# Kernel optimization log

Hardware: AMD Instinct MI355X
Metric: run time of the kernel (lower is better)

## Reference

```python
import jax, jax.numpy as jnp
import numpy as np

EPS = 1e-8


def setup_inputs() -> dict:
    key = jax.random.key(0)
    ks = jax.random.split(key, 3)
    B, d_in, d_sae = 2048, 2048, 16384
    x = jax.random.normal(ks[0], (B, 2, d_in), dtype=jnp.float32)
    W_enc = jax.random.normal(ks[1], (d_in, d_sae), dtype=jnp.float32) / (d_in ** 0.5)
    W_dec = jax.random.normal(ks[2], (d_sae, d_in), dtype=jnp.float32) / (d_sae ** 0.5)
    b_enc = jnp.zeros((d_sae,), dtype=jnp.float32)
    b_dec = jnp.zeros((d_in,), dtype=jnp.float32)
    return {"x": x, "W_enc": W_enc, "W_dec": W_dec, "b_enc": b_enc,
            "b_dec": b_dec, "k": 64, "h": 8192}


def _encode(x, W_enc, b_enc, k):
    # x: (N, d_in) -> z: (N, d_sae), top-k sparsified with relu on kept values
    pre = x @ W_enc + b_enc
    v, i = jax.lax.top_k(pre, k)                       # (N, k)
    rows = jnp.arange(pre.shape[0])[:, None]
    return jnp.zeros_like(pre).at[rows, i].set(jax.nn.relu(v))


def _info_nce(z_a, z_b):
    z_a = z_a / jnp.maximum(jnp.linalg.norm(z_a, axis=-1, keepdims=True), EPS)
    z_b = z_b / jnp.maximum(jnp.linalg.norm(z_b, axis=-1, keepdims=True), EPS)
    sim = z_a @ z_b.T                                  # (B, B)
    diag = jnp.diagonal(sim)
    ce_row = jnp.mean(jax.nn.logsumexp(sim, axis=1) - diag)
    ce_col = jnp.mean(jax.nn.logsumexp(sim, axis=0) - diag)
    return 0.5 * (ce_row + ce_col)


def reference(x, W_enc, W_dec, b_enc, b_dec, k, h):
    alpha = 1.0
    B, _, d_in = x.shape
    # encode both tokens in one GEMM: (2B, d_in)
    x_flat = x.reshape(B * 2, d_in)
    z = _encode(x_flat, W_enc, b_enc, k)               # (2B, d_sae)
    x_hat_full = z @ W_dec + b_dec                     # (2B, d_in)
    x_hat_high = z[:, :h] @ W_dec[:h, :] + b_dec       # (2B, d_in)
    per_tok = d_in
    # mean over batch per token, summed over prev+cur (matches 4 separate means)
    se_full = jnp.sum((x_hat_full - x_flat) ** 2, axis=-1).reshape(B, 2)
    se_high = jnp.sum((x_hat_high - x_flat) ** 2, axis=-1).reshape(B, 2)
    l_matr = (jnp.mean(se_full, axis=0).sum() + jnp.mean(se_high, axis=0).sum()) / per_tok
    z2 = z.reshape(B, 2, -1)
    z_h_prev = z2[:, 0, :h]
    z_h_cur = z2[:, 1, :h]
    l_contr = _info_nce(z_h_cur, z_h_prev)
    total = l_matr + alpha * l_contr
    x_hat_cur = x_hat_full.reshape(B, 2, d_in)[:, 1]
    z_cur = z2[:, 1]
    return (total, x_hat_cur, z_cur)
```

## Files before the change

kernel.cpp:

```cpp
#include <hip/hip_runtime.h>
#include <hip/hip_bf16.h>
#include <math.h>

#define D_IN   2048
#define D_SAE  16384
#define NROWS  4096
#define KTOP   64
#define HDIM   8192
#define CHUNK  1024
#define EPSN   1e-8f
#define BANDW_F16 4e-3f
#define BANDW_F32 4e-4f
#define BANDCAP 512
#define NTILE   128
#define SEG     16
#define CAPT    (NTILE*SEG)
#define TH_CAND 2.0f

typedef unsigned short u16;
typedef unsigned char u8;
typedef _Float16 f16;
typedef __attribute__((ext_vector_type(8))) _Float16 f16x8;
typedef __attribute__((ext_vector_type(4))) _Float16 f16x4;
typedef __attribute__((ext_vector_type(8))) unsigned short u16x8;
typedef __attribute__((ext_vector_type(4))) float float4v;
typedef __attribute__((ext_vector_type(2))) float f32x2;

__device__ __forceinline__ unsigned f2u(float f) {
  unsigned b = __float_as_uint(f);
  return (b & 0x80000000u) ? ~b : (b | 0x80000000u);
}
__device__ __forceinline__ float u2f(unsigned u) {
  unsigned b = (u & 0x80000000u) ? (u & 0x7fffffffu) : ~u;
  return __uint_as_float(b);
}
__device__ __forceinline__ u16 f2bf_rne(float f) {
  unsigned b = __float_as_uint(f);
  unsigned r = (b + 0x7fffu + ((b >> 16) & 1u)) >> 16;
  return (u16)r;
}
__device__ __forceinline__ float bf2f(u16 u) {
  return __uint_as_float(((unsigned)u) << 16);
}
__device__ __forceinline__ void async_copy16(void* lds, const void* g) {
  __builtin_amdgcn_global_load_lds(
      (const __attribute__((address_space(1))) unsigned*)(g),
      (__attribute__((address_space(3))) unsigned*)(lds), 16, 0, 0);
}

__global__ __launch_bounds__(256)
void pre_kernel(const float* __restrict__ x, const float* __restrict__ W,
                f16* __restrict__ Axh, f16* __restrict__ Th,
                float* __restrict__ WT)
{
  __shared__ float S[64][65];
  const int bid = blockIdx.x;
  if (bid < 8192) {
    const int tx = threadIdx.x & 63, ty = threadIdx.x >> 6;
    const int n0 = (bid & 255) * 64, k0 = (bid >> 8) * 64;
#pragma unroll
    for (int i = 0; i < 16; ++i) {
      int kl = ty + i * 4;
      S[kl][tx] = W[(size_t)(k0 + kl) * D_SAE + n0 + tx];
    }
    __syncthreads();
#pragma unroll
    for (int i = 0; i < 16; ++i) {
      int nl = ty + i * 4;
      float v = S[tx][nl];
      Th[(size_t)(n0 + nl) * D_IN + k0 + tx] = (f16)v;
      WT[(size_t)(n0 + nl) * D_IN + k0 + tx] = v;
    }
  } else {
    int t = (bid - 8192) * 256 + threadIdx.x;
    const int n4 = (NROWS * D_IN) / 4;
    if (t < n4) {
      float4 v = ((const float4*)x)[t];
      f16x4 h;
      h.x = (f16)v.x; h.y = (f16)v.y; h.z = (f16)v.z; h.w = (f16)v.w;
      ((f16x4*)Axh)[t] = h;
    }
  }
}

__global__ __launch_bounds__(512, 2)
void gemm_f16_kernel(const f16* __restrict__ Axh,
                     const f16* __restrict__ BT,
                     const float* __restrict__ bias,
                     unsigned* __restrict__ ckey_g,
                     u16* __restrict__ cidx_g,
                     unsigned* __restrict__ ccnt)
{
  __shared__ u16 As[2][2][256 * 32];
  __shared__ u16 Bs[2][2][256 * 32];
  const int tid  = threadIdx.x;
  const int wave = tid >> 6, lane = tid & 63;
  const int bid  = blockIdx.x;
  const int xcd  = bid & 7, loc = bid >> 3;
  const int n0   = (xcd * 8 + (loc >> 4)) * 256;
  const int m0   = (loc & 15) * 256;
  const int wr   = wave >> 2;
  const int wc   = wave & 3;
  const int fr   = lane & 15;
  const int fsl  = lane >> 4;

  float4v acc[8][4];
#pragma unroll
  for (int i = 0; i < 8; ++i)
#pragma unroll
    for (int j = 0; j < 4; ++j) acc[i][j] = (float4v){0.f, 0.f, 0.f, 0.f};

  int aoff[8], boff[4];
#pragma unroll
  for (int mi = 0; mi < 8; ++mi) {
    int row = wr * 128 + mi * 16 + fr;
    aoff[mi] = row * 32 + ((fsl ^ ((row >> 1) & 3)) * 8);
  }
#pragma unroll
  for (int n = 0; n < 4; ++n) {
    int col = wc * 64 + n * 16 + fr;
    boff[n] = col * 32 + ((fsl ^ ((col >> 1) & 3)) * 8);
  }

  auto stA = [&](int bf, int tt, int ks, int half) {
    int idx = half * 512 + tid;
    int row = idx >> 2, sl = idx & 3;
    int gc = tt * 64 + ks * 32 + ((sl ^ ((row >> 1) & 3)) * 8);
    async_copy16((char*)&As[bf][ks][0] + (size_t)idx * 16,
                 Axh + (size_t)(m0 + row) * D_IN + gc);
  };
  auto stB = [&](int bf, int tt, int ks, int half) {
    int idx = half * 512 + tid;
    int row = idx >> 2, sl = idx & 3;
    int gc = tt * 64 + ks * 32 + ((sl ^ ((row >> 1) & 3)) * 8);
    async_copy16((char*)&Bs[bf][ks][0] + (size_t)idx * 16,
                 BT + (size_t)(n0 + row) * D_IN + gc);
  };

  stA(0, 0, 0, 0); stA(0, 0, 0, 1); stB(0, 0, 0, 0); stB(0, 0, 0, 1);
  stA(0, 0, 1, 0); stA(0, 0, 1, 1); stB(0, 0, 1, 0); stB(0, 0, 1, 1);
  asm volatile("s_waitcnt vmcnt(4)" ::: "memory");
  __builtin_amdgcn_s_barrier();

  for (int t = 0; t < 32; ++t) {
    const int buf = t & 1, nbf = buf ^ 1;
    const bool st = (t < 31);
#pragma unroll
    for (int ks = 0; ks < 2; ++ks) {
      const u16* Ak = &As[buf][ks][0];
      const u16* Bk = &Bs[buf][ks][0];
      f16x8 b0 = *(const f16x8*)&Bk[boff[0]];
      f16x8 b1 = *(const f16x8*)&Bk[boff[1]];
      f16x8 b2 = *(const f16x8*)&Bk[boff[2]];
      f16x8 b3 = *(const f16x8*)&Bk[boff[3]];
      f16x8 a0 = *(const f16x8*)&Ak[aoff[0]];
      f16x8 a1 = *(const f16x8*)&Ak[aoff[1]];
      f16x8 a2 = *(const f16x8*)&Ak[aoff[2]];
      f16x8 a3 = *(const f16x8*)&Ak[aoff[3]];
      if (st) { stA(nbf, t + 1, ks, 0); stA(nbf, t + 1, ks, 1); }
      __builtin_amdgcn_s_setprio(1);
      acc[0][0] = __builtin_amdgcn_mfma_f32_16x16x32_f16(a0, b0, acc[0][0], 0, 0, 0);
      acc[0][1] = __builtin_amdgcn_mfma_f32_16x16x32_f16(a0, b1, acc[0][1], 0, 0, 0);
      acc[0][2] = __builtin_amdgcn_mfma_f32_16x16x32_f16(a0, b2, acc[0][2], 0, 0, 0);
      acc[0][3] = __builtin_amdgcn_mfma_f32_16x16x32_f16(a0, b3, acc[0][3], 0, 0, 0);
      acc[1][0] = __builtin_amdgcn_mfma_f32_16x16x32_f16(a1, b0, acc[1][0], 0, 0, 0);
      acc[1][1] = __builtin_amdgcn_mfma_f32_16x16x32_f16(a1, b1, acc[1][1], 0, 0, 0);
      acc[1][2] = __builtin_amdgcn_mfma_f32_16x16x32_f16(a1, b2, acc[1][2], 0, 0, 0);
      acc[1][3] = __builtin_amdgcn_mfma_f32_16x16x32_f16(a1, b3, acc[1][3], 0, 0, 0);
      acc[2][0] = __builtin_amdgcn_mfma_f32_16x16x32_f16(a2, b0, acc[2][0], 0, 0, 0);
      acc[2][1] = __builtin_amdgcn_mfma_f32_16x16x32_f16(a2, b1, acc[2][1], 0, 0, 0);
      acc[2][2] = __builtin_amdgcn_mfma_f32_16x16x32_f16(a2, b2, acc[2][2], 0, 0, 0);
      acc[2][3] = __builtin_amdgcn_mfma_f32_16x16x32_f16(a2, b3, acc[2][3], 0, 0, 0);
      acc[3][0] = __builtin_amdgcn_mfma_f32_16x16x32_f16(a3, b0, acc[3][0], 0, 0, 0);
      acc[3][1] = __builtin_amdgcn_mfma_f32_16x16x32_f16(a3, b1, acc[3][1], 0, 0, 0);
      acc[3][2] = __builtin_amdgcn_mfma_f32_16x16x32_f16(a3, b2, acc[3][2], 0, 0, 0);
      acc[3][3] = __builtin_amdgcn_mfma_f32_16x16x32_f16(a3, b3, acc[3][3], 0, 0, 0);
      __builtin_amdgcn_s_setprio(0);
      a0 = *(const f16x8*)&Ak[aoff[4]];
      a1 = *(const f16x8*)&Ak[aoff[5]];
      a2 = *(const f16x8*)&Ak[aoff[6]];
      a3 = *(const f16x8*)&Ak[aoff[7]];
      if (st) { stB(nbf, t + 1, ks, 0); stB(nbf, t + 1, ks, 1); }
      __builtin_amdgcn_s_setprio(1);
      acc[4][0] = __builtin_amdgcn_mfma_f32_16x16x32_f16(a0, b0, acc[4][0], 0, 0, 0);
      acc[4][1] = __builtin_amdgcn_mfma_f32_16x16x32_f16(a0, b1, acc[4][1], 0, 0, 0);
      acc[4][2] = __builtin_amdgcn_mfma_f32_16x16x32_f16(a0, b2, acc[4][2], 0, 0, 0);
      acc[4][3] = __builtin_amdgcn_mfma_f32_16x16x32_f16(a0, b3, acc[4][3], 0, 0, 0);
      acc[5][0] = __builtin_amdgcn_mfma_f32_16x16x32_f16(a1, b0, acc[5][0], 0, 0, 0);
      acc[5][1] = __builtin_amdgcn_mfma_f32_16x16x32_f16(a1, b1, acc[5][1], 0, 0, 0);
      acc[5][2] = __builtin_amdgcn_mfma_f32_16x16x32_f16(a1, b2, acc[5][2], 0, 0, 0);
      acc[5][3] = __builtin_amdgcn_mfma_f32_16x16x32_f16(a1, b3, acc[5][3], 0, 0, 0);
      acc[6][0] = __builtin_amdgcn_mfma_f32_16x16x32_f16(a2, b0, acc[6][0], 0, 0, 0);
      acc[6][1] = __builtin_amdgcn_mfma_f32_16x16x32_f16(a2, b1, acc[6][1], 0, 0, 0);
      acc[6][2] = __builtin_amdgcn_mfma_f32_16x16x32_f16(a2, b2, acc[6][2], 0, 0, 0);
      acc[6][3] = __builtin_amdgcn_mfma_f32_16x16x32_f16(a2, b3, acc[6][3], 0, 0, 0);
      acc[7][0] = __builtin_amdgcn_mfma_f32_16x16x32_f16(a3, b0, acc[7][0], 0, 0, 0);
      acc[7][1] = __builtin_amdgcn_mfma_f32_16x16x32_f16(a3, b1, acc[7][1], 0, 0, 0);
      acc[7][2] = __builtin_amdgcn_mfma_f32_16x16x32_f16(a3, b2, acc[7][2], 0, 0, 0);
      acc[7][3] = __builtin_amdgcn_mfma_f32_16x16x32_f16(a3, b3, acc[7][3], 0, 0, 0);
      __builtin_amdgcn_s_setprio(0);
      if (st) {
        asm volatile("s_waitcnt vmcnt(4)" ::: "memory");
        __builtin_amdgcn_s_barrier();
      } else if (ks == 0) {
        asm volatile("s_waitcnt vmcnt(0)" ::: "memory");
        __builtin_amdgcn_s_barrier();
      }
    }
  }
  __syncthreads();

  unsigned* lcnt = (unsigned*)&As[0][0][0];
  lcnt[tid] = 0u;
  __syncthreads();
  const int tl = wc >> 1;
  const int tileG = (n0 >> 7) + tl;
  const int orow = (lane >> 4) * 4;
#pragma unroll
  for (int mi = 0; mi < 8; ++mi) {
#pragma unroll
    for (int nj = 0; nj < 4; ++nj) {
      int col = n0 + wc * 64 + nj * 16 + fr;
      float bv = bias[col];
#pragma unroll
      for (int rr = 0; rr < 4; ++rr) {
        float val = acc[mi][nj][rr] + bv;
        if (val >= TH_CAND) {
          int lrow = wr * 128 + mi * 16 + orow + rr;
          unsigned j = atomicAdd(&lcnt[tl * 256 + lrow], 1u);
          if (j < SEG) {
            size_t sb = ((size_t)(m0 + lrow) * NTILE + tileG) * SEG;
            ckey_g[sb + j] = f2u(val);
            cidx_g[sb + j] = (u16)col;
          }
        }
      }
    }
  }
  __syncthreads();
  ccnt[(size_t)(m0 + (tid & 255)) * NTILE + (n0 >> 7) + (tid >> 8)] = lcnt[tid];
}

__global__ __launch_bounds__(256)
void select_compact_kernel(const unsigned* __restrict__ ckey_g,
                           const u16* __restrict__ cidx_g,
                           const unsigned* __restrict__ ccnt,
                           const float* __restrict__ x,
                           const float* __restrict__ WT,
                           const float* __restrict__ benc,
                           float bandw,
                           int*   __restrict__ topk_idx,
                           float* __restrict__ topk_val,
                           float* __restrict__ nh_norm,
                           unsigned* __restrict__ flags)
{
  __shared__ unsigned ckey[CAPT];
  __shared__ u16      cidx[CAPT];
  __shared__ unsigned tof[128];
  __shared__ unsigned tc[128];
  __shared__ unsigned hist[256];
  __shared__ unsigned sscan[257];
  __shared__ unsigned wsum[4];
  __shared__ float    bv_l[64];
  __shared__ int      band_idx[BANDCAP];
  __shared__ float    band_val[BANDCAP];
  __shared__ double   band_ex[BANDCAP];
  __shared__ unsigned char picked[BANDCAP];
  __shared__ int      out_idx[64];
  __shared__ float    out_val[64];
  __shared__ float    sh_v64;
  __shared__ unsigned sh_mcnt, sh_bstar, sh_kth, sh_ocnt, sh_bcnt, sh_bad;

  const int tid = threadIdx.x;
  const int wv = tid >> 6, ln = tid & 63;
  const int r = blockIdx.x;

  if (tid == 0) { sh_ocnt = 0u; sh_bcnt = 0u; sh_bad = 0u; sh_mcnt = 0u; sh_bstar = 0xffffffffu; }
  hist[tid] = 0u;
  if (tid < 128) {
    unsigned c = ccnt[(size_t)r * NTILE + tid];
    tc[tid] = c;
    if (c > SEG) sh_bad = 1u;
  }
  __syncthreads();
  if (tid < 128) {
    unsigned v = tc[tid];
#pragma unroll
    for (int d = 1; d < 64; d <<= 1) {
      unsigned t = __shfl_up(v, d);
      if (ln >= d) v += t;
    }
    tof[tid] = v;
  }
  __syncthreads();
  if (tid >= 64 && tid < 128) tof[tid] += tof[63];
  __syncthreads();
  const unsigned cc_u = tof[127];
  const int cc = (int)(cc_u < CAPT ? cc_u : CAPT);

  {
    unsigned ck[8]; u16 ci[8]; unsigned pv[8];
#pragma unroll
    for (int b = 0; b < 8; ++b) {
      int idx = tid + 256 * b;
      int tile = idx >> 4, slot = idx & 15;
      unsigned c = tc[tile]; if (c > SEG) c = SEG;
      bool valid = (unsigned)slot < c;
      pv[b] = valid ? (tof[tile] - tc[tile] + slot) : 0xffffffffu;
      ck[b] = valid ? ckey_g[(size_t)r * CAPT + idx] : 0u;
      ci[b] = valid ? cidx_g[(size_t)r * CAPT + idx] : (u16)0;
    }
#pragma unroll
    for (int b = 0; b < 8; ++b) {
      if (pv[b] < (unsigned)CAPT) { ckey[pv[b]] = ck[b]; cidx[pv[b]] = ci[b]; }
    }
  }
  __syncthreads();

  bool bad = (sh_bad != 0u) || (cc_u < 64u) || (cc_u > (unsigned)CAPT);

  if (!bad) {
    for (int s = tid; s < cc; s += 256) {
      float v = u2f(ckey[s]);
      int b = (int)((v - TH_CAND) * 100.0f);
      b = b < 0 ? 0 : (b > 255 ? 255 : b);
      atomicAdd(&hist[b], 1u);
    }
  }
  __syncthreads();
  {
    int rt = 255 - tid;
    unsigned v = hist[rt];
#pragma unroll
    for (int d = 1; d < 64; d <<= 1) {
      unsigned t = __shfl_up(v, d);
      if (ln >= d) v += t;
    }
    if (ln == 63) wsum[wv] = v;
    __syncthreads();
    unsigned add = 0;
    for (int w = 0; w < wv; ++w) add += wsum[w];
    sscan[rt] = v + add;
    if (tid == 0) sscan[256] = 0u;
    __syncthreads();
    if (sscan[tid] >= 64u && sscan[tid + 1] < 64u) {
      sh_bstar = (unsigned)tid;
      sh_kth = 64u - sscan[tid + 1];
    }
  }
  __syncthreads();

  if (bad || sh_bstar == 0xffffffffu) { if (tid == 0) flags[r] = 1u; return; }
  const int bstar = (int)sh_bstar;
  const unsigned kth = sh_kth;

  for (int s = tid; s < cc; s += 256) {
    float v = u2f(ckey[s]);
    int b = (int)((v - TH_CAND) * 100.0f);
    b = b < 0 ? 0 : (b > 255 ? 255 : b);
    if (b == bstar) {
      unsigned p = atomicAdd(&sh_mcnt, 1u);
      if (p < 64u) bv_l[p] = v;
    }
  }
  __syncthreads();
  if (sh_mcnt > 64u) { if (tid == 0) flags[r] = 1u; return; }
  const int m = (int)sh_mcnt;
  if (wv == 0 && ln < m) {
    float mine = bv_l[ln];
    int rank = 0;
    for (int j = 0; j < m; ++j) {
      float o = bv_l[j];
      if (o > mine || (o == mine && j < ln)) ++rank;
    }
    if (rank == (int)kth - 1) sh_v64 = mine;
  }
  __syncthreads();
  const float v64 = sh_v64;

  const float hi = v64 + 2.f * bandw, lo = v64 - 2.f * bandw;
  for (int s = tid; s < cc; s += 256) {
    float v = u2f(ckey[s]);
    int i = (int)cidx[s];
    if (v > hi) {
      unsigned p = atomicAdd(&sh_ocnt, 1u);
      out_idx[p] = i; out_val[p] = v;
    } else if (v >= lo) {
      unsigned p = atomicAdd(&sh_bcnt, 1u);
      if (p < BANDCAP) { band_idx[p] = i; band_val[p] = v; }
    }
  }
  __syncthreads();
  if (sh_bcnt > BANDCAP) { if (tid == 0) flags[r] = 1u; return; }
  const unsigned nci = sh_ocnt;
  const unsigned bcnt = sh_bcnt;
  const unsigned remaining = 64u - nci;

  if (bcnt == remaining) {
    for (unsigned s = tid; s < bcnt; s += 256) {
      out_idx[nci + s] = band_idx[s];
      out_val[nci + s] = band_val[s];
    }
    __syncthreads();
  } else {
    const float* xr = x + (size_t)r * 2048;
    for (unsigned bi = wv; bi < bcnt; bi += 4) {
      int c = band_idx[bi];
      const float* wr = WT + (size_t)c * 2048;
      double s = 0.0;
      for (int j0 = 0; j0 < 2048; j0 += 512) {
        float xa[8], wa[8];
#pragma unroll
        for (int u = 0; u < 8; ++u) {
          int j = j0 + ln + 64 * u;
          xa[u] = xr[j];
          wa[u] = wr[j];
        }
#pragma unroll
        for (int u = 0; u < 8; ++u)
          s += (double)xa[u] * (double)wa[u];
      }
#pragma unroll
      for (int off2 = 32; off2 > 0; off2 >>= 1)
        s += __shfl_down(s, off2);
      if (ln == 0) band_ex[bi] = s + (double)benc[c];
    }
    __syncthreads();
    if (tid == 0) {
      for (unsigned i2 = 0; i2 < bcnt; ++i2) picked[i2] = 0;
      for (unsigned s = 0; s < remaining; ++s) {
        int best = -1;
        for (unsigned b2 = 0; b2 < bcnt; ++b2) {
          if (picked[b2]) continue;
          if (best < 0 || band_ex[b2] > band_ex[best] ||
              (band_ex[b2] == band_ex[best] && band_idx[b2] < band_idx[best]))
            best = (int)b2;
        }
        picked[best] = 1;
        out_idx[nci + s] = band_idx[best];
        out_val[nci + s] = (float)band_ex[best];
      }
    }
    __syncthreads();
  }

  if (tid < 64) {
    float v = out_val[tid];
    v = v > 0.f ? v : 0.f;
    out_val[tid] = v;
    topk_idx[(size_t)r * 64 + tid] = out_idx[tid];
    topk_val[(size_t)r * 64 + tid] = v;
  }
  __syncthreads();
  if (tid == 0) {
    float n2 = 0.f;
    for (int s = 0; s < 64; ++s)
      if (out_idx[s] < HDIM) n2 += out_val[s] * out_val[s];
    nh_norm[r] = sqrtf(n2);
    flags[r] = 0u;
  }
}

__global__ __launch_bounds__(256)
void repair_kernel(const unsigned* __restrict__ flags,
                   const float* __restrict__ x,
                   const float* __restrict__ WT,
                   const float* __restrict__ benc,
                   int* __restrict__ topk_idx,
                   float* __restrict__ topk_val,
                   float* __restrict__ nh_norm)
{
  const int r = blockIdx.x;
  if (flags[r] == 0u) return;
  __shared__ float prerow[16384];
  __shared__ float xs[2048];
  __shared__ float rv[256];
  __shared__ int   ri[256];
  __shared__ int   oi[64];
  __shared__ float ov[64];
  const int tid = threadIdx.x;
  for (int i = tid; i < 2048; i += 256) xs[i] = x[(size_t)r * 2048 + i];
  __syncthreads();
  for (int c = tid; c < 16384; c += 256) {
    const float* wr = WT + (size_t)c * 2048;
    float s = 0.f;
    for (int j = 0; j < 2048; ++j) s = fmaf(xs[j], wr[j], s);
    prerow[c] = s + benc[c];
  }
  __syncthreads();
  for (int k2 = 0; k2 < 64; ++k2) {
    float bv = -INFINITY; int bi = 16384;
    for (int c = tid; c < 16384; c += 256) {
      float v = prerow[c];
      if (v > bv || (v == bv && c < bi)) { bv = v; bi = c; }
    }
    rv[tid] = bv; ri[tid] = bi;
    __syncthreads();
    for (int s2 = 128; s2 > 0; s2 >>= 1) {
      if (tid < s2) {
        if (rv[tid+s2] > rv[tid] || (rv[tid+s2] == rv[tid] && ri[tid+s2] < ri[tid])) {
          rv[tid] = rv[tid+s2]; ri[tid] = ri[tid+s2];
        }
      }
      __syncthreads();
    }
    if (tid == 0) { oi[k2] = ri[0]; ov[k2] = rv[0]; prerow[ri[0]] = -INFINITY; }
    __syncthreads();
  }
  if (tid < 64) {
    float v = ov[tid]; v = v > 0.f ? v : 0.f;
    topk_idx[(size_t)r * 64 + tid] = oi[tid];
    topk_val[(size_t)r * 64 + tid] = v;
  }
  __syncthreads();
  if (tid == 0) {
    float n2 = 0.f;
    for (int s = 0; s < 64; ++s)
      if (oi[s] < HDIM) { float v = ov[s] > 0.f ? ov[s] : 0.f; n2 += v * v; }
    nh_norm[r] = sqrtf(n2);
  }
}

__global__ __launch_bounds__(256)
void wdec_scatter_kernel(const float* __restrict__ W,
                         u8* __restrict__ W8, float* __restrict__ scl,
                         const int* __restrict__ topk_idx,
                         const float* __restrict__ topk_val,
                         const float* __restrict__ nh_norm,
                         u16* __restrict__ ZpTb)
{
  const int bid = blockIdx.x;
  const int tid = threadIdx.x;
  if (bid < 16384) {
    __shared__ float red[256];
    const int c = bid;
    const int e0 = tid * 8;
    const float* wr = W + (size_t)c * 2048;
    float4 a = *(const float4*)(wr + e0);
    float4 b = *(const float4*)(wr + e0 + 4);
    float w[8] = {a.x,a.y,a.z,a.w,b.x,b.y,b.z,b.w};
    float mx = 0.f;
#pragma unroll
    for (int i = 0; i < 8; ++i) mx = fmaxf(mx, fabsf(w[i]));
    red[tid] = mx; __syncthreads();
    for (int s = 128; s > 0; s >>= 1) { if (tid < s) red[tid] = fmaxf(red[tid], red[tid+s]); __syncthreads(); }
    const float mxa = red[0];
    const float senc = mxa > 0.f ? 448.f / mxa : 0.f;
    float q[8];
#pragma unroll
    for (int i = 0; i < 8; ++i) q[i] = fminf(fmaxf(w[i] * senc, -448.f), 448.f);
    int p0 = __builtin_amdgcn_cvt_pk_fp8_f32(q[0], q[1], 0, false);
    p0 = __builtin_amdgcn_cvt_pk_fp8_f32(q[2], q[3], p0, true);
    int p1 = __builtin_amdgcn_cvt_pk_fp8_f32(q[4], q[5], 0, false);
    p1 = __builtin_amdgcn_cvt_pk_fp8_f32(q[6], q[7], p1, true);
    uint2 o; o.x = (unsigned)p0; o.y = (unsigned)p1;
    *(uint2*)(W8 + (size_t)c * 2048 + e0) = o;
    if (tid == 0) scl[c] = mxa > 0.f ? mxa / 448.f : 0.f;
  } else {
    int t = (bid - 16384) * 256 + tid;
    if (t < 2048 * 64) {
      int b = t >> 6;
      int r = 2 * b;
      int c = topk_idx[(size_t)r * 64 + (t & 63)];
      float v = topk_val[(size_t)r * 64 + (t & 63)];
      if (c < HDIM) {
        float nrm = nh_norm[r]; nrm = nrm > EPSN ? nrm : EPSN;
        ZpTb[(size_t)c * 2048 + b] = f2bf_rne(v / nrm);
      }
    }
  }
}

__global__ __launch_bounds__(256)
void token_kernel(const int* __restrict__ topk_idx,
                  const float* __restrict__ topk_val,
                  const u8* __restrict__ W8,
                  const float* __restrict__ scl,
                  const float* __restrict__ bdec,
                  const float* __restrict__ x,
                  const float* __restrict__ nh_norm,
                  const u16* __restrict__ ZpTb,
                  float* __restrict__ se_full,
                  float* __restrict__ se_high,
                  float* __restrict__ xhat_out,
                  float* __restrict__ zcur_out,
                  float* __restrict__ simb,
                  float* __restrict__ lse_row,
                  float* __restrict__ diag)
{
  __shared__ int sidx[64];
  __shared__ float sval[64];
  __shared__ float rawv[64];
  __shared__ float red[256];
  __shared__ int cidx2[64];
  __shared__ float cval2[64];
  __shared__ u8 zmap[16384];
  __shared__ int scnt;
  const int tid = threadIdx.x;
  const int r = blockIdx.x;
  const int e0 = tid * 8;
  const bool odd = (r & 1);
  if (tid == 0) scnt = 0;
  if (odd) {
    unsigned* zm = (unsigned*)zmap;
#pragma unroll
    for (int j = 0; j < 16; ++j) zm[tid + 256 * j] = 0xFFFFFFFFu;
  }
  if (tid < 64) {
    int c = topk_idx[(size_t)r*64+tid];
    float v = topk_val[(size_t)r*64+tid];
    sidx[tid] = c;
    rawv[tid] = v;
    sval[tid] = v * scl[c];
  }
  __syncthreads();
  if (odd && tid < 64) zmap[sidx[tid]] = (u8)tid;
  float accf[8], acch[8];
  {
    float4 b0 = *(const float4*)(bdec + e0);
    float4 b1 = *(const float4*)(bdec + e0 + 4);
    accf[0]=b0.x; accf[1]=b0.y; accf[2]=b0.z; accf[3]=b0.w;
    accf[4]=b1.x; accf[5]=b1.y; accf[6]=b1.z; accf[7]=b1.w;
#pragma unroll
    for (int i = 0; i < 8; ++i) acch[i] = accf[i];
  }
  for (int s0 = 0; s0 < 64; s0 += 8) {
    uint2 w[8]; float vf[8], vh[8];
#pragma unroll
    for (int j = 0; j < 8; ++j) {
      int c = sidx[s0 + j];
      float v = sval[s0 + j];
      vf[j] = v;
      vh[j] = (c < HDIM) ? v : 0.f;
      w[j] = *(const uint2*)(W8 + (size_t)c * 2048 + e0);
    }
#pragma unroll
    for (int j = 0; j < 8; ++j) {
      f32x2 f0 = __builtin_amdgcn_cvt_pk_f32_fp8((int)w[j].x, false);
      f32x2 f1 = __builtin_amdgcn_cvt_pk_f32_fp8((int)w[j].x, true);
      f32x2 f2 = __builtin_amdgcn_cvt_pk_f32_fp8((int)w[j].y, false);
      f32x2 f3 = __builtin_amdgcn_cvt_pk_f32_fp8((int)w[j].y, true);
      float wvv[8] = {f0[0],f0[1],f1[0],f1[1],f2[0],f2[1],f3[0],f3[1]};
#pragma unroll
      for (int i = 0; i < 8; ++i) {
        accf[i] = fmaf(vf[j], wvv[i], accf[i]);
        acch[i] = fmaf(vh[j], wvv[i], acch[i]);
      }
    }
  }
  const float* xr = x + (size_t)r * 2048;
  float4 x0 = *(const float4*)(xr + e0);
  float4 x1 = *(const float4*)(xr + e0 + 4);
  float xv[8] = {x0.x,x0.y,x0.z,x0.w,x1.x,x1.y,x1.z,x1.w};
  float sf = 0.f, shs = 0.f;
#pragma unroll
  for (int i = 0; i < 8; ++i) {
    float df = accf[i] - xv[i]; sf += df*df;
    float dh = acch[i] - xv[i]; shs += dh*dh;
  }
  red[tid] = sf; __syncthreads();
  for (int s2=128; s2>0; s2>>=1){ if (tid<s2) red[tid]+=red[tid+s2]; __syncthreads(); }
  if (tid==0) se_full[r] = red[0];
  __syncthreads();
  red[tid] = shs; __syncthreads();
  for (int s2=128; s2>0; s2>>=1){ if (tid<s2) red[tid]+=red[tid+s2]; __syncthreads(); }
  if (tid==0) se_high[r] = red[0];
  if (!odd) return;

  {
    float* orow = xhat_out + (size_t)(r >> 1) * 2048;
    float4 o0 = {accf[0],accf[1],accf[2],accf[3]};
    float4 o1 = {accf[4],accf[5],accf[6],accf[7]};
    *(float4*)(orow + e0) = o0;
    *(float4*)(orow + e0 + 4) = o1;
  }
  {
    float* zrow = zcur_out + (size_t)(r >> 1) * 16384;
#pragma unroll
    for (int it = 0; it < 16; ++it) {
      int c0 = it * 1024 + tid * 4;
      float4 o;
      u8 s0m = zmap[c0 + 0]; o.x = (s0m < 64) ? rawv[s0m] : 0.f;
      u8 s1m = zmap[c0 + 1]; o.y = (s1m < 64) ? rawv[s1m] : 0.f;
      u8 s2m = zmap[c0 + 2]; o.z = (s2m < 64) ? rawv[s2m] : 0.f;
      u8 s3m = zmap[c0 + 3]; o.w = (s3m < 64) ? rawv[s3m] : 0.f;
      *(float4*)(zrow + c0) = o;
    }
  }
  const int i = r >> 1;
  __syncthreads();
  if (tid < 64) {
    int c = sidx[tid];
    float v = rawv[tid];
    if (c < HDIM) {
      float nrm = nh_norm[r]; nrm = nrm > EPSN ? nrm : EPSN;
      int p = atomicAdd(&scnt, 1);
      cidx2[p] = c; cval2[p] = v / nrm;
    }
  }
  __syncthreads();
  float acc[8];
#pragma unroll
  for (int ii = 0; ii < 8; ++ii) acc[ii] = 0.f;
  const int m = scnt;
  int s = 0;
  for (; s + 8 <= m; s += 8) {
    u16x8 z[8]; float vv[8];
#pragma unroll
    for (int j = 0; j < 8; ++j) {
      vv[j] = cval2[s + j];
      z[j] = *(const u16x8*)(ZpTb + (size_t)cidx2[s + j] * 2048 + e0);
    }
#pragma unroll
    for (int j = 0; j < 8; ++j)
#pragma unroll
      for (int ii = 0; ii < 8; ++ii)
        acc[ii] = fmaf(vv[j], bf2f(z[j][ii]), acc[ii]);
  }
  for (; s < m; ++s) {
    int c = cidx2[s]; float v = cval2[s];
    u16x8 z8 = *(const u16x8*)(ZpTb + (size_t)c * 2048 + e0);
#pragma unroll
    for (int ii = 0; ii < 8; ++ii)
      acc[ii] = fmaf(v, bf2f(z8[ii]), acc[ii]);
  }
  {
    float* srow = simb + (size_t)i * 2048;
    float4 o0 = {acc[0],acc[1],acc[2],acc[3]};
    float4 o1 = {acc[4],acc[5],acc[6],acc[7]};
    *(float4*)(srow + e0) = o0;
    *(float4*)(srow + e0 + 4) = o1;
  }
  float mx = -INFINITY;
#pragma unroll
  for (int ii = 0; ii < 8; ++ii) mx = fmaxf(mx, acc[ii]);
  if ((i >> 3) == tid) diag[i] = acc[i & 7];
  red[tid] = mx; __syncthreads();
  for (int s2=128; s2>0; s2>>=1){ if (tid<s2) red[tid]=fmaxf(red[tid],red[tid+s2]); __syncthreads(); }
  mx = red[0]; __syncthreads();
  float se = 0.f;
#pragma unroll
  for (int ii = 0; ii < 8; ++ii) se += expf(acc[ii] - mx);
  red[tid] = se; __syncthreads();
  for (int s2=128; s2>0; s2>>=1){ if (tid<s2) red[tid]+=red[tid+s2]; __syncthreads(); }
  if (tid == 0) lse_row[i] = mx + logf(red[0]);
}

__global__ __launch_bounds__(256)
void gemm_pre_kernel(const float* __restrict__ A,
                     const float* __restrict__ B,
                     const float* __restrict__ bias,
                     float* __restrict__ C)
{
  __shared__ float As[16][129];
  __shared__ float Bs[16][129];
  const int tid = threadIdx.x;
  const int tx = tid & 15, ty = tid >> 4;
  const int m0 = blockIdx.y * 128;
  const int n0 = blockIdx.x * 128;
  float acc[8][8];
#pragma unroll
  for (int i = 0; i < 8; ++i)
#pragma unroll
    for (int j = 0; j < 8; ++j) acc[i][j] = 0.f;
  const int lk = tid & 15, lm = tid >> 4;
  for (int k0 = 0; k0 < 2048; k0 += 16) {
#pragma unroll
    for (int i = 0; i < 8; ++i) {
      int m = lm + 16 * i;
      As[lk][m] = A[(size_t)(m0 + m) * 2048 + k0 + lk];
    }
#pragma unroll
    for (int i = 0; i < 8; ++i) {
      int idx = tid + 256 * i;
      int kk = idx >> 7, nn = idx & 127;
      Bs[kk][nn] = B[(size_t)(k0 + kk) * 16384 + n0 + nn];
    }
    __syncthreads();
#pragma unroll
    for (int kk = 0; kk < 16; ++kk) {
      float a[8], b[8];
#pragma unroll
      for (int i = 0; i < 8; ++i) a[i] = As[kk][ty + 16 * i];
#pragma unroll
      for (int j = 0; j < 8; ++j) b[j] = Bs[kk][tx + 16 * j];
#pragma unroll
      for (int i = 0; i < 8; ++i)
#pragma unroll
        for (int j = 0; j < 8; ++j) acc[i][j] = fmaf(a[i], b[j], acc[i][j]);
    }
    __syncthreads();
  }
#pragma unroll
  for (int i = 0; i < 8; ++i) {
    int m = m0 + ty + 16 * i;
#pragma unroll
    for (int j = 0; j < 8; ++j) {
      int n = n0 + tx + 16 * j;
      C[(size_t)m * 16384 + n] = acc[i][j] + bias[n];
    }
  }
}

__global__ __launch_bounds__(256)
void select_fb_kernel(const float* __restrict__ pre,
                      const float* __restrict__ x,
                      const float* __restrict__ Wenc,
                      const float* __restrict__ benc,
                      int row_base, float bandw,
                      int*   __restrict__ topk_idx,
                      float* __restrict__ topk_val,
                      float* __restrict__ nh_norm)
{
  __shared__ unsigned hist[256];
  __shared__ int      band_idx[BANDCAP];
  __shared__ double   band_ex[BANDCAP];
  __shared__ double   red_d[256];
  __shared__ int      out_idx[64];
  __shared__ float    out_val[64];
  __shared__ unsigned char picked[BANDCAP];
  __shared__ unsigned sh_prefix, sh_need, sh_ocnt, sh_bcnt;

  const int tid = threadIdx.x;
  const int lrow = blockIdx.x;
  const int row = row_base + lrow;
  const float* prow = pre + (size_t)lrow * 16384;

  if (tid == 0) { sh_prefix = 0u; sh_need = 64u; }
  __syncthreads();
  for (int level = 24; level >= 0; level -= 8) {
    hist[tid] = 0u;
    __syncthreads();
    unsigned prefix = sh_prefix;
    for (int i = tid; i < 16384; i += 256) {
      unsigned u = f2u(prow[i]);
      bool match = (level == 24) || ((u >> ((level + 8) & 31)) == prefix);
      if (match) atomicAdd(&hist[(u >> level) & 255u], 1u);
    }
    __syncthreads();
    if (tid == 0) {
      unsigned need = sh_need, acc = 0; int q = 0;
      for (int b2 = 255; b2 >= 0; --b2) {
        if (acc + hist[b2] >= need) { q = b2; break; }
        acc += hist[b2];
      }
      sh_prefix = (prefix << 8) | (unsigned)q;
      sh_need = need - acc;
    }
    __syncthreads();
  }
  const float v64 = u2f(sh_prefix);

  if (tid == 0) { sh_ocnt = 0u; sh_bcnt = 0u; }
  __syncthreads();
  const float hi = v64 + 2.f * bandw, lo = v64 - 2.f * bandw;
  for (int i = tid; i < 16384; i += 256) {
    float v = prow[i];
    if (v > hi) {
      unsigned p = atomicAdd(&sh_ocnt, 1u);
      out_idx[p] = i; out_val[p] = v;
    } else if (v >= lo) {
      unsigned p = atomicAdd(&sh_bcnt, 1u);
      if (p < BANDCAP) { band_idx[p] = i; }
    }
  }
  __syncthreads();
  const unsigned nci = sh_ocnt;
  const unsigned bcnt = sh_bcnt < BANDCAP ? sh_bcnt : BANDCAP;
  const unsigned remaining = 64u - nci;

  if (bcnt == remaining) {
    for (unsigned s = tid; s < bcnt; s += 256) {
      int c = band_idx[s];
      out_idx[nci + s] = c;
      out_val[nci + s] = prow[c];
    }
    __syncthreads();
  } else {
    const float* xr = x + (size_t)row * 2048;
    for (unsigned bi = 0; bi < bcnt; ++bi) {
      int c = band_idx[bi];
      double part = 0.0;
#pragma unroll
      for (int j2 = 0; j2 < 8; ++j2) {
        int kk = tid + 256 * j2;
        part += (double)xr[kk] * (double)Wenc[(size_t)kk * 16384 + c];
      }
      red_d[tid] = part;
      __syncthreads();
      for (int sft = 128; sft > 0; sft >>= 1) {
        if (tid < sft) red_d[tid] += red_d[tid + sft];
        __syncthreads();
      }
      if (tid == 0) band_ex[bi] = red_d[0] + (double)benc[c];
      __syncthreads();
    }
    if (tid == 0) {
      for (unsigned i2 = 0; i2 < bcnt; ++i2) picked[i2] = 0;
      for (unsigned s = 0; s < remaining; ++s) {
        int best = -1;
        for (unsigned b2 = 0; b2 < bcnt; ++b2) {
          if (picked[b2]) continue;
          if (best < 0 || band_ex[b2] > band_ex[best] ||
              (band_ex[b2] == band_ex[best] && band_idx[b2] < band_idx[best]))
            best = (int)b2;
        }
        picked[best] = 1;
        out_idx[nci + s] = band_idx[best];
        out_val[nci + s] = (float)band_ex[best];
      }
    }
    __syncthreads();
  }

  if (tid < 64) {
    float v = out_val[tid];
    v = v > 0.f ? v : 0.f;
    out_val[tid] = v;
    topk_idx[(size_t)row * 64 + tid] = out_idx[tid];
    topk_val[(size_t)row * 64 + tid] = v;
  }
  __syncthreads();
  if (tid == 0) {
    float n2 = 0.f;
    for (int s = 0; s < 64; ++s)
      if (out_idx[s] < HDIM) n2 += out_val[s] * out_val[s];
    nh_norm[row] = sqrtf(n2);
  }
}

__global__ __launch_bounds__(256)
void scatter_f32_kernel(const int* __restrict__ topk_idx,
                        const float* __restrict__ topk_val,
                        const float* __restrict__ nh_norm,
                        float* __restrict__ zcur_out,
                        float* __restrict__ ZpT)
{
  int t = blockIdx.x * blockDim.x + threadIdx.x;
  if (t >= NROWS * 64) return;
  int r = t >> 6;
  int c = topk_idx[t];
  float v = topk_val[t];
  int b = r >> 1;
  if (r & 1) {
    zcur_out[(size_t)b * 16384 + c] = v;
  } else if (c < HDIM) {
    float nrm = nh_norm[r]; nrm = nrm > EPSN ? nrm : EPSN;
    ZpT[(size_t)c * 2048 + b] = v / nrm;
  }
}

__global__ __launch_bounds__(256)
void decode_f32_kernel(const int* __restrict__ topk_idx,
                       const float* __restrict__ topk_val,
                       const float* __restrict__ Wdec,
                       const float* __restrict__ bdec,
                       const float* __restrict__ x,
                       float* __restrict__ se_full,
                       float* __restrict__ se_high,
                       float* __restrict__ xhat_out)
{
  __shared__ int sidx[64];
  __shared__ float sval[64];
  __shared__ float red[256];
  const int tid = threadIdx.x;
  const int r = blockIdx.x;
  if (tid < 64) { sidx[tid] = topk_idx[(size_t)r*64+tid]; sval[tid] = topk_val[(size_t)r*64+tid]; }
  __syncthreads();
  float accf[8], acch[8];
#pragma unroll
  for (int i = 0; i < 8; ++i) { float b = bdec[tid + 256*i]; accf[i] = b; acch[i] = b; }
  for (int s = 0; s < 64; ++s) {
    int c = sidx[s]; float v = sval[s];
    const float* wr = Wdec + (size_t)c * 2048;
    bool high = (c < HDIM);
#pragma unroll
    for (int i = 0; i < 8; ++i) {
      float w = wr[tid + 256*i];
      accf[i] = fmaf(v, w, accf[i]);
      if (high) acch[i] = fmaf(v, w, acch[i]);
    }
  }
  const float* xr = x + (size_t)r * 2048;
  float sf = 0.f, shs = 0.f;
#pragma unroll
  for (int i = 0; i < 8; ++i) {
    float xv = xr[tid + 256*i];
    float df = accf[i] - xv; sf += df*df;
    float dh = acch[i] - xv; shs += dh*dh;
  }
  red[tid] = sf; __syncthreads();
  for (int s2=128; s2>0; s2>>=1){ if (tid<s2) red[tid]+=red[tid+s2]; __syncthreads(); }
  if (tid==0) se_full[r] = red[0];
  __syncthreads();
  red[tid] = shs; __syncthreads();
  for (int s2=128; s2>0; s2>>=1){ if (tid<s2) red[tid]+=red[tid+s2]; __syncthreads(); }
  if (tid==0) se_high[r] = red[0];
  if (r & 1) {
    float* orow = xhat_out + (size_t)(r >> 1) * 2048;
#pragma unroll
    for (int i = 0; i < 8; ++i) orow[tid + 256*i] = accf[i];
  }
}

__global__ __launch_bounds__(256)
void sim_f32_kernel(const int* __restrict__ topk_idx,
                    const float* __restrict__ topk_val,
                    const float* __restrict__ nh_norm,
                    const float* __restrict__ ZpT,
                    float* __restrict__ sim)
{
  __shared__ int cidx2[64];
  __shared__ float cval2[64];
  __shared__ int scnt;
  const int tid = threadIdx.x;
  const int i = blockIdx.x;
  const int r = 2 * i + 1;
  if (tid == 0) scnt = 0;
  __syncthreads();
  if (tid < 64) {
    int c = topk_idx[(size_t)r*64+tid];
    float v = topk_val[(size_t)r*64+tid];
    if (c < HDIM) {
      float nrm = nh_norm[r]; nrm = nrm > EPSN ? nrm : EPSN;
      int p = atomicAdd(&scnt, 1);
      cidx2[p] = c; cval2[p] = v / nrm;
    }
  }
  __syncthreads();
  float acc[8];
#pragma unroll
  for (int ii = 0; ii < 8; ++ii) acc[ii] = 0.f;
  int m = scnt;
  for (int s = 0; s < m; ++s) {
    int c = cidx2[s]; float v = cval2[s];
    const float* zr = ZpT + (size_t)c * 2048;
#pragma unroll
    for (int ii = 0; ii < 8; ++ii)
      acc[ii] = fmaf(v, zr[tid + 256*ii], acc[ii]);
  }
  float* srow = sim + (size_t)i * 2048;
#pragma unroll
  for (int ii = 0; ii < 8; ++ii) srow[tid + 256*ii] = acc[ii];
}

__global__ __launch_bounds__(256)
void lse_row_kernel(const float* __restrict__ sim,
                    float* __restrict__ lse_row, float* __restrict__ diag)
{
  __shared__ float red[256];
  const int tid = threadIdx.x; const int i = blockIdx.x;
  const int e0 = tid * 8;
  const float* srow = sim + (size_t)i * 2048;
  float4 v0 = *(const float4*)(srow + e0);
  float4 v1 = *(const float4*)(srow + e0 + 4);
  float vals[8] = {v0.x,v0.y,v0.z,v0.w,v1.x,v1.y,v1.z,v1.w};
  float mx = -INFINITY;
#pragma unroll
  for (int ii=0; ii<8; ++ii) mx = fmaxf(mx, vals[ii]);
  if ((i >> 3) == tid) diag[i] = vals[i & 7];
  red[tid]=mx; __syncthreads();
  for (int s=128;s>0;s>>=1){ if (tid<s) red[tid]=fmaxf(red[tid],red[tid+s]); __syncthreads(); }
  mx = red[0]; __syncthreads();
  float se=0.f;
#pragma unroll
  for (int ii=0;ii<8;++ii) se += expf(vals[ii]-mx);
  red[tid]=se; __syncthreads();
  for (int s=128;s>0;s>>=1){ if (tid<s) red[tid]+=red[tid+s]; __syncthreads(); }
  if (tid==0) lse_row[i] = mx + logf(red[0]);
}

__global__ __launch_bounds__(256)
void lse_col_kernel(const float* __restrict__ sim, float* __restrict__ lse_col)
{
  __shared__ float ml[32][9], sl[32][9];
  const int tid = threadIdx.x;
  const int c = tid & 7, rr = tid >> 3;
  const int col = blockIdx.x * 8 + c;
  float m = -INFINITY, s = 0.f;
  for (int r = rr; r < 2048; r += 32) {
    float v = sim[(size_t)r * 2048 + col];
    float mn = fmaxf(m, v);
    s = s * expf(m - mn) + expf(v - mn);
    m = mn;
  }
  ml[rr][c] = m; sl[rr][c] = s;
  __syncthreads();
  if (rr == 0) {
    float M = ml[0][c];
#pragma unroll
    for (int i = 1; i < 32; ++i) M = fmaxf(M, ml[i][c]);
    float S = 0.f;
#pragma unroll
    for (int i = 0; i < 32; ++i) S += sl[i][c] * expf(ml[i][c] - M);
    lse_col[col] = M + logf(S);
  }
}

__global__ __launch_bounds__(256)
void final_kernel(const float* __restrict__ se_full, const float* __restrict__ se_high,
                  const float* __restrict__ lse_row, const float* __restrict__ lse_col,
                  const float* __restrict__ diag, float* __restrict__ out0)
{
  __shared__ float red[256];
  const int tid = threadIdx.x;
  float s1 = 0.f;
  for (int i = tid; i < 4096; i += 256) s1 += se_full[i] + se_high[i];
  red[tid]=s1; __syncthreads();
  for (int s=128;s>0;s>>=1){ if (tid<s) red[tid]+=red[tid+s]; __syncthreads(); }
  float matr = red[0]; __syncthreads();
  float s2 = 0.f;
  for (int i = tid; i < 2048; i += 256) s2 += (lse_row[i]-diag[i]) + (lse_col[i]-diag[i]);
  red[tid]=s2; __syncthreads();
  for (int s=128;s>0;s>>=1){ if (tid<s) red[tid]+=red[tid+s]; __syncthreads(); }
  if (tid == 0) {
    float l_matr  = matr / (2048.f * 2048.f);
    float l_contr = 0.5f * (red[0] / 2048.f);
    out0[0] = l_matr + l_contr;
  }
}

extern "C" void kernel_launch(void* const* d_in, const int* in_sizes, int n_in,
                              void* d_out, int out_size, void* d_ws, size_t ws_size,
                              hipStream_t stream)
{
  const float* x    = (const float*)d_in[0];
  const float* Wenc = (const float*)d_in[1];
  const float* Wdec = (const float*)d_in[2];
  const float* benc = (const float*)d_in[3];
  const float* bdec = (const float*)d_in[4];
  float* out = (float*)d_out;
  float* xhat_out = out + 1;
  float* zcur_out = out + 1 + (size_t)2048 * 2048;
  (void)in_sizes; (void)n_in; (void)out_size;

  char* ws = (char*)d_ws;
  size_t off = 0;
  auto alloc = [&](size_t bytes) {
    char* p = ws + off; off += (bytes + 255) & ~(size_t)255; return p;
  };
  int*      tki     = (int*)     alloc((size_t)NROWS * 64 * 4);
  float*    tkv     = (float*)   alloc((size_t)NROWS * 64 * 4);
  float*    nh_norm = (float*)   alloc((size_t)NROWS * 4);
  float*    se_f    = (float*)   alloc((size_t)NROWS * 4);
  float*    se_h    = (float*)   alloc((size_t)NROWS * 4);
  float*    lse_r   = (float*)   alloc((size_t)2048 * 4);
  float*    lse_c   = (float*)   alloc((size_t)2048 * 4);
  float*    diag    = (float*)   alloc((size_t)2048 * 4);
  f16*      Axh     = (f16*)     alloc((size_t)NROWS * D_IN * 2);
  unsigned* ckey_g  = (unsigned*)alloc((size_t)NROWS * CAPT * 4);
  u16*      cidx_g  = (u16*)     alloc((size_t)NROWS * CAPT * 2);
  unsigned* ccnt    = (unsigned*)alloc((size_t)NROWS * NTILE * 4);
  unsigned* flags   = (unsigned*)alloc((size_t)NROWS * 4);
  char*     R1      = alloc((size_t)D_SAE * D_IN * 2);
  char*     R2      = alloc((size_t)D_SAE * D_IN * 4);
  size_t need = off;

  f16*   Th    = (f16*)R1;
  u8*    W8    = (u8*)R1;
  float* scl   = (float*)(R1 + (size_t)D_SAE * D_IN);
  float* WT    = (float*)R2;
  u16*   ZpTb  = (u16*)R2;
  float* simb  = (float*)(R2 + (size_t)8192 * 2048 * 2);

  if (ws_size >= need) {
    pre_kernel<<<16384, 256, 0, stream>>>(x, Wenc, Axh, Th, WT);
    gemm_f16_kernel<<<1024, 512, 0, stream>>>(Axh, Th, benc, ckey_g, cidx_g, ccnt);
    select_compact_kernel<<<NROWS, 256, 0, stream>>>(ckey_g, cidx_g, ccnt, x, WT, benc,
        BANDW_F16, tki, tkv, nh_norm, flags);
    repair_kernel<<<NROWS, 256, 0, stream>>>(flags, x, WT, benc, tki, tkv, nh_norm);
    hipMemsetAsync(ZpTb, 0, (size_t)8192 * 2048 * 2, stream);
    wdec_scatter_kernel<<<16384 + 512, 256, 0, stream>>>(Wdec, W8, scl,
        tki, tkv, nh_norm, ZpTb);
    token_kernel<<<NROWS, 256, 0, stream>>>(tki, tkv, W8, scl, bdec, x, nh_norm, ZpTb,
        se_f, se_h, xhat_out, zcur_out, simb, lse_r, diag);
    lse_col_kernel<<<256, 256, 0, stream>>>(simb, lse_c);
    final_kernel<<<1, 256, 0, stream>>>(se_f, se_h, lse_r, lse_c, diag, out);
  } else {
    off = 0;
    float* pre2  = (float*)alloc((size_t)CHUNK * 16384 * 4);
    int*   tki2  = (int*)  alloc((size_t)NROWS * 64 * 4);
    float* tkv2  = (float*)alloc((size_t)NROWS * 64 * 4);
    float* nh2   = (float*)alloc((size_t)NROWS * 4);
    float* sef2  = (float*)alloc((size_t)NROWS * 4);
    float* seh2  = (float*)alloc((size_t)NROWS * 4);
    float* lr2   = (float*)alloc((size_t)2048 * 4);
    float* lc2   = (float*)alloc((size_t)2048 * 4);
    float* dg2   = (float*)alloc((size_t)2048 * 4);
    float* ZpT2  = (float*)alloc((size_t)8192 * 2048 * 4);
    float* sim2  = (float*)alloc((size_t)2048 * 2048 * 4);
    hipMemsetAsync(zcur_out, 0, (size_t)2048 * 16384 * 4, stream);
    for (int ch = 0; ch < 4; ++ch) {
      dim3 g(128, 8);
      gemm_pre_kernel<<<g, 256, 0, stream>>>(x + (size_t)ch * CHUNK * 2048, Wenc, benc, pre2);
      select_fb_kernel<<<CHUNK, 256, 0, stream>>>(pre2, x, Wenc, benc,
          ch * CHUNK, BANDW_F32, tki2, tkv2, nh2);
    }
    hipMemsetAsync(ZpT2, 0, (size_t)8192 * 2048 * 4, stream);
    scatter_f32_kernel<<<(NROWS * 64) / 256, 256, 0, stream>>>(tki2, tkv2, nh2, zcur_out, ZpT2);
    decode_f32_kernel<<<NROWS, 256, 0, stream>>>(tki2, tkv2, Wdec, bdec, x, sef2, seh2, xhat_out);
    sim_f32_kernel<<<2048, 256, 0, stream>>>(tki2, tkv2, nh2, ZpT2, sim2);
    lse_row_kernel<<<2048, 256, 0, stream>>>(sim2, lr2, dg2);
    lse_col_kernel<<<256, 256, 0, stream>>>(sim2, lc2);
    final_kernel<<<1, 256, 0, stream>>>(sef2, seh2, lr2, lc2, dg2, out);
  }
}
```

Measured before the change: 684.8 us.

## Restructure f16 encoder GEMM into 8-wave ping-pong schedule with BK=64 tiles

```diff
diff --git a/kernel.cpp b/kernel.cpp
--- a/kernel.cpp
+++ b/kernel.cpp
@@ -83,7 +83,7 @@
   }
 }
 
-__global__ __launch_bounds__(512, 2)
+__global__ __launch_bounds__(512, 1)
 void gemm_f16_kernel(const f16* __restrict__ Axh,
                      const f16* __restrict__ BT,
                      const float* __restrict__ bias,
@@ -91,8 +91,8 @@
                      u16* __restrict__ cidx_g,
                      unsigned* __restrict__ ccnt)
 {
-  __shared__ u16 As[2][2][256 * 32];
-  __shared__ u16 Bs[2][2][256 * 32];
+  __shared__ u16 As[2][2][128 * 64];
+  __shared__ u16 Bs[2][2][128 * 64];
   const int tid  = threadIdx.x;
   const int wave = tid >> 6, lane = tid & 63;
   const int bid  = blockIdx.x;
@@ -110,103 +110,121 @@
 #pragma unroll
     for (int j = 0; j < 4; ++j) acc[i][j] = (float4v){0.f, 0.f, 0.f, 0.f};
 
-  int aoff[8], boff[4];
-#pragma unroll
-  for (int mi = 0; mi < 8; ++mi) {
-    int row = wr * 128 + mi * 16 + fr;
-    aoff[mi] = row * 32 + ((fsl ^ ((row >> 1) & 3)) * 8);
-  }
-#pragma unroll
-  for (int n = 0; n < 4; ++n) {
-    int col = wc * 64 + n * 16 + fr;
-    boff[n] = col * 32 + ((fsl ^ ((col >> 1) & 3)) * 8);
-  }
-
-  auto stA = [&](int bf, int tt, int ks, int half) {
-    int idx = half * 512 + tid;
-    int row = idx >> 2, sl = idx & 3;
-    int gc = tt * 64 + ks * 32 + ((sl ^ ((row >> 1) & 3)) * 8);
-    async_copy16((char*)&As[bf][ks][0] + (size_t)idx * 16,
-                 Axh + (size_t)(m0 + row) * D_IN + gc);
+  int aofs[2][4][2], bofs[2][2][2];
+#pragma unroll
+  for (int mhq = 0; mhq < 2; ++mhq)
+#pragma unroll
+    for (int mi = 0; mi < 4; ++mi)
+#pragma unroll
+      for (int kk = 0; kk < 2; ++kk) {
+        int rl = mhq * 64 + mi * 16 + fr;
+        aofs[mhq][mi][kk] = rl * 64 + (((kk * 4 + fsl) ^ (rl & 7)) * 8);
+      }
+#pragma unroll
+  for (int nhq = 0; nhq < 2; ++nhq)
+#pragma unroll
+    for (int nj = 0; nj < 2; ++nj)
+#pragma unroll
+      for (int kk = 0; kk < 2; ++kk) {
+        int cl = (wc & 1) * 64 + nhq * 32 + nj * 16 + fr;
+        bofs[nhq][nj][kk] = cl * 64 + (((kk * 4 + fsl) ^ (cl & 7)) * 8);
+      }
+
+  f16x8 a[4][2], b[2][2][2];
+
+  auto rdA = [&](int d, int mhq) {
+#pragma unroll
+    for (int mi = 0; mi < 4; ++mi)
+#pragma unroll
+      for (int kk = 0; kk < 2; ++kk)
+        a[mi][kk] = *(const f16x8*)&As[d][wr][aofs[mhq][mi][kk]];
   };
-  auto stB = [&](int bf, int tt, int ks, int half) {
-    int idx = half * 512 + tid;
-    int row = idx >> 2, sl = idx & 3;
-    int gc = tt * 64 + ks * 32 + ((sl ^ ((row >> 1) & 3)) * 8);
-    async_copy16((char*)&Bs[bf][ks][0] + (size_t)idx * 16,
-                 BT + (size_t)(n0 + row) * D_IN + gc);
+  auto rdB = [&](int d, int nhq) {
+#pragma unroll
+    for (int nj = 0; nj < 2; ++nj)
+#pragma unroll
+      for (int kk = 0; kk < 2; ++kk)
+        b[nhq][nj][kk] = *(const f16x8*)&Bs[d][wc >> 1][bofs[nhq][nj][kk]];
   };
-
-  stA(0, 0, 0, 0); stA(0, 0, 0, 1); stB(0, 0, 0, 0); stB(0, 0, 0, 1);
-  stA(0, 0, 1, 0); stA(0, 0, 1, 1); stB(0, 0, 1, 0); stB(0, 0, 1, 1);
-  asm volatile("s_waitcnt vmcnt(4)" ::: "memory");
+  auto domfma = [&](int mhq, int nhq) {
+    __builtin_amdgcn_s_setprio(1);
+#pragma unroll
+    for (int mi = 0; mi < 4; ++mi)
+#pragma unroll
+      for (int nj = 0; nj < 2; ++nj)
+#pragma unroll
+        for (int kk = 0; kk < 2; ++kk)
+          acc[mhq*4+mi][nhq*2+nj] = __builtin_amdgcn_mfma_f32_16x16x32_f16(
+              a[mi][kk], b[nhq][nj][kk], acc[mhq*4+mi][nhq*2+nj], 0, 0, 0);
+    __builtin_amdgcn_s_setprio(0);
+  };
+  auto stage = [&](u16* base, const f16* grow, int tt) {
+#pragma unroll
+    for (int ig = 0; ig < 2; ++ig) {
+      int idx = ig * 512 + tid;
+      int rl = idx >> 3, sl = idx & 7;
+      int gc = tt * 64 + ((sl ^ (rl & 7)) * 8);
+      async_copy16((char*)base + (size_t)idx * 16,
+                   grow + (size_t)rl * D_IN + gc);
+    }
+  };
+  const f16* Ah0 = Axh + (size_t)m0 * D_IN;
+  const f16* Ah1 = Axh + (size_t)(m0 + 128) * D_IN;
+  const f16* Bh0 = BT + (size_t)n0 * D_IN;
+  const f16* Bh1 = BT + (size_t)(n0 + 128) * D_IN;
+
+  stage(&As[0][0][0], Ah0, 0); stage(&As[0][1][0], Ah1, 0);
+  stage(&Bs[0][0][0], Bh0, 0); stage(&Bs[0][1][0], Bh1, 0);
+  stage(&Bs[1][0][0], Bh0, 1); stage(&Bs[1][1][0], Bh1, 1);
+  asm volatile("s_waitcnt vmcnt(0)" ::: "memory");
   __builtin_amdgcn_s_barrier();
 
-  for (int t = 0; t < 32; ++t) {
-    const int buf = t & 1, nbf = buf ^ 1;
-    const bool st = (t < 31);
-#pragma unroll
-    for (int ks = 0; ks < 2; ++ks) {
-      const u16* Ak = &As[buf][ks][0];
-      const u16* Bk = &Bs[buf][ks][0];
-      f16x8 b0 = *(const f16x8*)&Bk[boff[0]];
-      f16x8 b1 = *(const f16x8*)&Bk[boff[1]];
-      f16x8 b2 = *(const f16x8*)&Bk[boff[2]];
-      f16x8 b3 = *(const f16x8*)&Bk[boff[3]];
-      f16x8 a0 = *(const f16x8*)&Ak[aoff[0]];
-      f16x8 a1 = *(const f16x8*)&Ak[aoff[1]];
-      f16x8 a2 = *(const f16x8*)&Ak[aoff[2]];
-      f16x8 a3 = *(const f16x8*)&Ak[aoff[3]];
-      if (st) { stA(nbf, t + 1, ks, 0); stA(nbf, t + 1, ks, 1); }
-      __builtin_amdgcn_s_setprio(1);
-      acc[0][0] = __builtin_amdgcn_mfma_f32_16x16x32_f16(a0, b0, acc[0][0], 0, 0, 0);
-      acc[0][1] = __builtin_amdgcn_mfma_f32_16x16x32_f16(a0, b1, acc[0][1], 0, 0, 0);
-      acc[0][2] = __builtin_amdgcn_mfma_f32_16x16x32_f16(a0, b2, acc[0][2], 0, 0, 0);
-      acc[0][3] = __builtin_amdgcn_mfma_f32_16x16x32_f16(a0, b3, acc[0][3], 0, 0, 0);
-      acc[1][0] = __builtin_amdgcn_mfma_f32_16x16x32_f16(a1, b0, acc[1][0], 0, 0, 0);
-      acc[1][1] = __builtin_amdgcn_mfma_f32_16x16x32_f16(a1, b1, acc[1][1], 0, 0, 0);
-      acc[1][2] = __builtin_amdgcn_mfma_f32_16x16x32_f16(a1, b2, acc[1][2], 0, 0, 0);
-      acc[1][3] = __builtin_amdgcn_mfma_f32_16x16x32_f16(a1, b3, acc[1][3], 0, 0, 0);
-      acc[2][0] = __builtin_amdgcn_mfma_f32_16x16x32_f16(a2, b0, acc[2][0], 0, 0, 0);
-      acc[2][1] = __builtin_amdgcn_mfma_f32_16x16x32_f16(a2, b1, acc[2][1], 0, 0, 0);
-      acc[2][2] = __builtin_amdgcn_mfma_f32_16x16x32_f16(a2, b2, acc[2][2], 0, 0, 0);
-      acc[2][3] = __builtin_amdgcn_mfma_f32_16x16x32_f16(a2, b3, acc[2][3], 0, 0, 0);
-      acc[3][0] = __builtin_amdgcn_mfma_f32_16x16x32_f16(a3, b0, acc[3][0], 0, 0, 0);
-      acc[3][1] = __builtin_amdgcn_mfma_f32_16x16x32_f16(a3, b1, acc[3][1], 0, 0, 0);
-      acc[3][2] = __builtin_amdgcn_mfma_f32_16x16x32_f16(a3, b2, acc[3][2], 0, 0, 0);
-      acc[3][3] = __builtin_amdgcn_mfma_f32_16x16x32_f16(a3, b3, acc[3][3], 0, 0, 0);
-      __builtin_amdgcn_s_setprio(0);
-      a0 = *(const f16x8*)&Ak[aoff[4]];
-      a1 = *(const f16x8*)&Ak[aoff[5]];
-      a2 = *(const f16x8*)&Ak[aoff[6]];
-      a3 = *(const f16x8*)&Ak[aoff[7]];
-      if (st) { stB(nbf, t + 1, ks, 0); stB(nbf, t + 1, ks, 1); }
-      __builtin_amdgcn_s_setprio(1);
-      acc[4][0] = __builtin_amdgcn_mfma_f32_16x16x32_f16(a0, b0, acc[4][0], 0, 0, 0);
-      acc[4][1] = __builtin_amdgcn_mfma_f32_16x16x32_f16(a0, b1, acc[4][1], 0, 0, 0);
-      acc[4][2] = __builtin_amdgcn_mfma_f32_16x16x32_f16(a0, b2, acc[4][2], 0, 0, 0);
-      acc[4][3] = __builtin_amdgcn_mfma_f32_16x16x32_f16(a0, b3, acc[4][3], 0, 0, 0);
-      acc[5][0] = __builtin_amdgcn_mfma_f32_16x16x32_f16(a1, b0, acc[5][0], 0, 0, 0);
-      acc[5][1] = __builtin_amdgcn_mfma_f32_16x16x32_f16(a1, b1, acc[5][1], 0, 0, 0);
-      acc[5][2] = __builtin_amdgcn_mfma_f32_16x16x32_f16(a1, b2, acc[5][2], 0, 0, 0);
-      acc[5][3] = __builtin_amdgcn_mfma_f32_16x16x32_f16(a1, b3, acc[5][3], 0, 0, 0);
-      acc[6][0] = __builtin_amdgcn_mfma_f32_16x16x32_f16(a2, b0, acc[6][0], 0, 0, 0);
-      acc[6][1] = __builtin_amdgcn_mfma_f32_16x16x32_f16(a2, b1, acc[6][1], 0, 0, 0);
-      acc[6][2] = __builtin_amdgcn_mfma_f32_16x16x32_f16(a2, b2, acc[6][2], 0, 0, 0);
-      acc[6][3] = __builtin_amdgcn_mfma_f32_16x16x32_f16(a2, b3, acc[6][3], 0, 0, 0);
-      acc[7][0] = __builtin_amdgcn_mfma_f32_16x16x32_f16(a3, b0, acc[7][0], 0, 0, 0);
-      acc[7][1] = __builtin_amdgcn_mfma_f32_16x16x32_f16(a3, b1, acc[7][1], 0, 0, 0);
-      acc[7][2] = __builtin_amdgcn_mfma_f32_16x16x32_f16(a3, b2, acc[7][2], 0, 0, 0);
-      acc[7][3] = __builtin_amdgcn_mfma_f32_16x16x32_f16(a3, b3, acc[7][3], 0, 0, 0);
-      __builtin_amdgcn_s_setprio(0);
-      if (st) {
-        asm volatile("s_waitcnt vmcnt(4)" ::: "memory");
-        __builtin_amdgcn_s_barrier();
-      } else if (ks == 0) {
-        asm volatile("s_waitcnt vmcnt(0)" ::: "memory");
-        __builtin_amdgcn_s_barrier();
-      }
-    }
+#pragma unroll 1
+  for (int j = 0; j < 16; ++j) {
+    const int t1 = 2 * j + 1, t2 = 2 * j + 2, t3 = 2 * j + 3;
+    const bool g = (j < 15);
+    rdA(0, 0); rdB(0, 0);
+    stage(&As[1][0][0], Ah0, t1);
+    __builtin_amdgcn_s_barrier();
+    domfma(0, 0);
+    __builtin_amdgcn_s_barrier();
+    rdB(0, 1);
+    stage(&As[1][1][0], Ah1, t1);
+    __builtin_amdgcn_s_barrier();
+    domfma(0, 1);
+    __builtin_amdgcn_s_barrier();
+    rdA(0, 1);
+    if (g) stage(&Bs[0][0][0], Bh0, t2);
+    __builtin_amdgcn_s_barrier();
+    domfma(1, 0);
+    __builtin_amdgcn_s_barrier();
+    if (g) stage(&Bs[0][1][0], Bh1, t2);
+    __builtin_amdgcn_s_barrier();
+    domfma(1, 1);
+    if (g) { asm volatile("s_waitcnt vmcnt(4)" ::: "memory"); }
+    else   { asm volatile("s_waitcnt vmcnt(0)" ::: "memory"); }
+    __builtin_amdgcn_s_barrier();
+    rdA(1, 0); rdB(1, 0);
+    if (g) stage(&As[0][0][0], Ah0, t2);
+    __builtin_amdgcn_s_barrier();
+    domfma(0, 0);
+    __builtin_amdgcn_s_barrier();
+    rdB(1, 1);
+    if (g) stage(&As[0][1][0], Ah1, t2);
+    __builtin_amdgcn_s_barrier();
+    domfma(0, 1);
+    __builtin_amdgcn_s_barrier();
+    rdA(1, 1);
+    if (g) stage(&Bs[1][0][0], Bh0, t3);
+    __builtin_amdgcn_s_barrier();
+    domfma(1, 0);
+    __builtin_amdgcn_s_barrier();
+    if (g) stage(&Bs[1][1][0], Bh1, t3);
+    __builtin_amdgcn_s_barrier();
+    domfma(1, 1);
+    if (g) { asm volatile("s_waitcnt vmcnt(4)" ::: "memory"); }
+    else   { asm volatile("s_waitcnt vmcnt(0)" ::: "memory"); }
+    __builtin_amdgcn_s_barrier();
   }
   __syncthreads();
 
@@ -220,13 +238,13 @@
   for (int mi = 0; mi < 8; ++mi) {
 #pragma unroll
     for (int nj = 0; nj < 4; ++nj) {
-      int col = n0 + wc * 64 + nj * 16 + fr;
+      int col = n0 + wc * 64 + (nj >> 1) * 32 + (nj & 1) * 16 + fr;
       float bv = bias[col];
 #pragma unroll
       for (int rr = 0; rr < 4; ++rr) {
         float val = acc[mi][nj][rr] + bv;
         if (val >= TH_CAND) {
-          int lrow = wr * 128 + mi * 16 + orow + rr;
+          int lrow = wr * 128 + (mi >> 2) * 64 + (mi & 3) * 16 + orow + rr;
           unsigned j = atomicAdd(&lcnt[tl * 256 + lrow], 1u);
           if (j < SEG) {
             size_t sb = ((size_t)(m0 + lrow) * NTILE + tileG) * SEG;
```

After: 643.8 us. 6.0% less time.
